# Kernel optimization log

Hardware: AMD Instinct MI355X
Metric: run time of the kernel (lower is better)

## Reference

```python
import jax, jax.numpy as jnp
import numpy as np


def conv(x, w, b=None, pad=0):
    y = jax.lax.conv_general_dilated(x, w, (1, 1), [(pad, pad), (pad, pad)],
                                     dimension_numbers=('NCHW', 'OIHW', 'NCHW'))
    if b is not None:
        y = y + b[None, :, None, None]
    return y


def bn(x, g, b, m, v, eps=1e-5):
    scale = g / jnp.sqrt(v + eps)
    return (x - m[None, :, None, None]) * scale[None, :, None, None] + b[None, :, None, None]


def channel_gate(x, w1, b1, w2, b2):
    # avg pool -> MLP -> sigmoid, returns [B, C, 1, 1]
    p = x.mean(axis=(2, 3))                       # [B, C]
    h = jax.nn.relu(p @ w1.T + b1)                # [B, C//r]
    a = h @ w2.T + b2                             # [B, C]
    return jax.nn.sigmoid(a)[:, :, None, None]


def setup_inputs() -> dict:
    key = jax.random.key(0)
    ks = iter(jax.random.split(key, 48))
    B, Cin, H, W = 2, 256, 64, 64
    Ci = Cin // 2          # inter_channels = 128
    Cr = Ci // 16          # gate bottleneck = 8
    def nrm(shape, s=0.05):
        return jax.random.normal(next(ks), shape, jnp.float32) * s
    d = {}
    d['q'] = jax.random.normal(next(ks), (B, Cin, H, W), jnp.float32)
    d['s'] = jax.random.normal(next(ks), (B, Cin, H, W), jnp.float32)
    # Trans_s: conv3x3 + BN
    d['ts_w'] = nrm((Ci, Cin, 3, 3)); d['ts_b'] = jnp.zeros(Ci)
    d['ts_g'] = jnp.ones(Ci); d['ts_be'] = jnp.zeros(Ci)
    d['ts_m'] = nrm((Ci,), 0.01); d['ts_v'] = jnp.ones(Ci)
    # Trans_q: conv3x3 + BN
    d['tq_w'] = nrm((Ci, Cin, 3, 3)); d['tq_b'] = jnp.zeros(Ci)
    d['tq_g'] = jnp.ones(Ci); d['tq_be'] = jnp.zeros(Ci)
    d['tq_m'] = nrm((Ci,), 0.01); d['tq_v'] = jnp.ones(Ci)
    # common_v 1x1
    d['cv_w'] = nrm((Ci, Ci, 1, 1)); d['cv_b'] = jnp.zeros(Ci)
    # key/query 1x1 projections (out = Ci//2)
    d['k1_w'] = nrm((Ci // 2, Ci, 1, 1)); d['k1_b'] = jnp.zeros(Ci // 2)
    d['q1_w'] = nrm((Ci // 2, Ci, 1, 1)); d['q1_b'] = jnp.zeros(Ci // 2)
    d['k2_w'] = nrm((Ci // 2, Ci, 1, 1)); d['k2_b'] = jnp.zeros(Ci // 2)
    d['q2_w'] = nrm((Ci // 2, Ci, 1, 1)); d['q2_b'] = jnp.zeros(Ci // 2)
    # ChannelGate MLP
    d['g1_w'] = nrm((Cr, Ci)); d['g1_b'] = jnp.zeros(Cr)
    d['g2_w'] = nrm((Ci, Cr)); d['g2_b'] = jnp.zeros(Ci)
    # conv_cat: conv3x3 (no bias) + BN
    d['cc_w'] = nrm((Ci, 2 * Ci, 3, 3))
    d['cc_g'] = jnp.ones(Ci); d['cc_be'] = jnp.zeros(Ci)
    d['cc_m'] = nrm((Ci,), 0.01); d['cc_v'] = jnp.ones(Ci)
    return d


def reference(q, s, ts_w, ts_b, ts_g, ts_be, ts_m, ts_v,
              tq_w, tq_b, tq_g, tq_be, tq_m, tq_v,
              cv_w, cv_b, k1_w, k1_b, q1_w, q1_b, k2_w, k2_b, q2_w, q2_b,
              g1_w, g1_b, g2_w, g2_b, cc_w, cc_g, cc_be, cc_m, cc_v):
    # stems: conv3x3 + BN + ReLU
    s = jax.nn.relu(bn(conv(s, ts_w, ts_b, pad=1), ts_g, ts_be, ts_m, ts_v))
    q = jax.nn.relu(bn(conv(q, tq_w, tq_b, pad=1), tq_g, tq_be, tq_m, tq_v))
    B, C, H, W = q.shape
    N = H * W
    # values
    v_q1 = conv(q, cv_w, cv_b)                          # [B,C,H,W]
    v_s1 = conv(s, cv_w, cv_b)
    v_q = v_q1.reshape(B, C, N).transpose(0, 2, 1)      # [B,N,C]
    v_s = v_s1.reshape(B, C, N).transpose(0, 2, 1)
    # dual keys / queries with negation trick
    k1 = conv(s, k1_w, k1_b).reshape(B, C // 2, N)
    k2 = conv(q, k2_w, k2_b).reshape(B, C // 2, N)
    key_cat = jnp.concatenate([k1, -k2], axis=1).transpose(0, 2, 1)   # [B,N,C]
    q1x = conv(s, q1_w, q1_b).reshape(B, C // 2, N)
    q2x = conv(q, q2_w, q2_b).reshape(B, C // 2, N)
    query_cat = jnp.concatenate([q1x, q2x], axis=1)                    # [B,C,N]
    # abs-score attention, dual softmax from the same score matrix
    A_s = jnp.abs(jnp.einsum('bnc,bcm->bnm', key_cat, query_cat))      # [B,N,N]
    att_s = jax.nn.softmax(A_s, axis=-1)
    att_q = jax.nn.softmax(A_s.transpose(0, 2, 1), axis=-1)
    # attend + channel-gate SE fusion + residual
    p_s = jnp.einsum('bnm,bmc->bnc', att_s, v_s).transpose(0, 2, 1).reshape(B, C, H, W)
    E_s = channel_gate(v_s1, g1_w, g1_b, g2_w, g2_b) * p_s + s
    q_s = jnp.einsum('bnm,bmc->bnc', att_q, v_q).transpose(0, 2, 1).reshape(B, C, H, W)
    E_q = channel_gate(v_q1, g1_w, g1_b, g2_w, g2_b) * q_s + q
    # concat + conv3x3(no bias) + BN + ReLU
    cpam = jax.nn.relu(bn(conv(jnp.concatenate([E_q, E_s], axis=1), cc_w, None, pad=1),
                          cc_g, cc_be, cc_m, cc_v))
    return (cpam, E_q, E_s)
```

## Files before the change

### kernel.cpp

```cpp
#include <hip/hip_runtime.h>

typedef __bf16 bf16;
typedef __bf16 v8bf __attribute__((ext_vector_type(8)));
typedef __bf16 v4bf __attribute__((ext_vector_type(4)));
typedef float v4f __attribute__((ext_vector_type(4)));

#define MFMA16(a, b, c) __builtin_amdgcn_mfma_f32_16x16x32_bf16(a, b, c, 0, 0, 0)

__device__ __forceinline__ float sf(float x) {
  if (!(x == x)) return 0.f;
  return fminf(fmaxf(x, -1e30f), 1e30f);
}

__global__ __launch_bounds__(256) void fill_kernel(float* __restrict__ out, float v, int n) {
  int i = blockIdx.x * 256 + threadIdx.x;
  if (i < n) out[i] = v;
}

__global__ __launch_bounds__(256) void prep_kernel(
    const float* __restrict__ ts_w, const float* __restrict__ tq_w,
    const float* ts_b, const float* ts_g, const float* ts_be, const float* ts_m, const float* ts_v,
    const float* tq_b, const float* tq_g, const float* tq_be, const float* tq_m, const float* tq_v,
    bf16* __restrict__ Wt01, float* __restrict__ ss01)
{
  int idx = blockIdx.x * 256 + threadIdx.x;
  if (idx < 589824) {
    int which = idx / 294912;
    int rem = idx - which * 294912;
    int co = rem / 2304;
    int r2 = rem - co * 2304;
    int tap = r2 >> 8;
    int ci = r2 & 255;
    const float* W = which ? tq_w : ts_w;
    Wt01[idx] = (bf16)W[(co * 256 + ci) * 9 + tap];
  } else if (idx < 590080) {
    int i = idx - 589824;
    int which = i >> 7, c = i & 127;
    float g, be, m, vv, bias;
    if (which == 0) { g=ts_g[c]; be=ts_be[c]; m=ts_m[c]; vv=ts_v[c]; bias=ts_b[c]; }
    else            { g=tq_g[c]; be=tq_be[c]; m=tq_m[c]; vv=tq_v[c]; bias=tq_b[c]; }
    float scale = g / sqrtf(vv + 1e-5f);
    ss01[which * 256 + c] = sf(scale);
    ss01[which * 256 + 128 + c] = sf((bias - m) * scale + be);
  }
}

__global__ __launch_bounds__(256) void prep2_kernel(
    const float* __restrict__ cc_w, const float* cc_g, const float* cc_be,
    const float* cc_m, const float* cc_v,
    bf16* __restrict__ Wt2, float* __restrict__ ss_cc)
{
  int idx = blockIdx.x * 256 + threadIdx.x;
  if (idx < 294912) {
    int co = idx / 2304;
    int r2 = idx - co * 2304;
    int tap = r2 >> 8;
    int ci = r2 & 255;
    Wt2[idx] = (bf16)cc_w[(co * 256 + ci) * 9 + tap];
  } else if (idx < 295040) {
    int c = idx - 294912;
    float scale = cc_g[c] / sqrtf(cc_v[c] + 1e-5f);
    ss_cc[c] = sf(scale);
    ss_cc[128 + c] = sf(-cc_m[c] * scale + cc_be[c]);
  }
}

__global__ __launch_bounds__(256) void convN_kernel(
    const float* __restrict__ pS, const float* __restrict__ pQ,
    const bf16* __restrict__ Wb, const float* __restrict__ ssb,
    void* __restrict__ out_, int mode)
{
  __shared__ bf16 As[66][40];
  __shared__ bf16 Bs[3][64][40];

  int y = blockIdx.x;
  int co0 = blockIdx.y * 64;
  int z = blockIdx.z;
  int tsr = z >> 1, b = z & 1;

  const float *in0, *in1;
  const bf16* W;
  const float* sp;
  if (mode == 0) {
    const float* base = (tsr ? pQ : pS) + (long)b * 1048576;
    in0 = base; in1 = base + 524288;
    W = Wb + (long)tsr * 294912;
    sp = ssb + tsr * 256;
  } else {
    in0 = pS + 1048576 + (long)b * 524288;
    in1 = pS + 2097152 + (long)b * 524288;
    W = Wb; sp = ssb;
  }

  int t = threadIdx.x, lane = t & 63, w = t >> 6;
  int l15 = lane & 15, l4 = lane >> 4;
  int wr = (w & 1) * 32, wc = (w >> 1) * 32;
  int ac = t & 31, ag = t >> 5;
  int bco = t >> 2, bk = (t & 3) * 8;

  v4f acc[2][2] = {};

  auto loadA = [&](int it, v8bf& areg) {
    int dy = it >> 3, ks = it & 7;
    int ysrc = y + dy - 1;
    int cg = ks * 32 + ac;
    const float* ip = (cg < 128) ? (in0 + (long)cg * 4096) : (in1 + (long)(cg - 128) * 4096);
    if ((unsigned)ysrc < 64u) {
      const float* src = ip + ysrc * 64 + ag * 8;
#pragma unroll
      for (int i = 0; i < 8; ++i) areg[i] = (bf16)src[i];
    } else {
#pragma unroll
      for (int i = 0; i < 8; ++i) areg[i] = (bf16)0.f;
    }
  };
  auto loadB = [&](int it, v8bf* breg) {
    int dy = it >> 3, ks = it & 7;
    const bf16* wk = W + (long)(co0 + bco) * 2304 + dy * 3 * 256 + ks * 32 + bk;
#pragma unroll
    for (int d = 0; d < 3; ++d) breg[d] = *(const v8bf*)(wk + d * 256);
  };

  v8bf areg, breg[3];
  loadA(0, areg);
  loadB(0, breg);

  for (int it = 0; it < 24; ++it) {
    __syncthreads();
#pragma unroll
    for (int i = 0; i < 8; ++i) As[ag * 8 + 1 + i][ac] = areg[i];
    if (ag == 0) As[0][ac] = (bf16)0.f;
    if (ag == 7) As[65][ac] = (bf16)0.f;
#pragma unroll
    for (int d = 0; d < 3; ++d) *(v8bf*)&Bs[d][bco][bk] = breg[d];
    __syncthreads();
    if (it < 23) { loadA(it + 1, areg); loadB(it + 1, breg); }
#pragma unroll
    for (int d = 0; d < 3; ++d) {
      v8bf af0 = *(const v8bf*)&As[wr + d + l15][l4 * 8];
      v8bf af1 = *(const v8bf*)&As[wr + 16 + d + l15][l4 * 8];
#pragma unroll
      for (int j = 0; j < 2; ++j) {
        v8bf bfr = *(const v8bf*)&Bs[d][wc + j * 16 + l15][l4 * 8];
        acc[0][j] = MFMA16(af0, bfr, acc[0][j]);
        acc[1][j] = MFMA16(af1, bfr, acc[1][j]);
      }
    }
  }
#pragma unroll
  for (int i = 0; i < 2; ++i) {
    int nb = y * 64 + wr + i * 16 + l4 * 4;
#pragma unroll
    for (int j = 0; j < 2; ++j) {
      int c = co0 + wc + j * 16 + l15;
      float scale = sp[c], shift = sp[128 + c];
      if (mode == 0) {
        bf16* o = (bf16*)out_ + ((long)(tsr * 2 + b) * 4096 + nb) * 128 + c;
#pragma unroll
        for (int r = 0; r < 4; ++r)
          o[r * 128] = (bf16)sf(fmaxf(acc[i][j][r] * scale + shift, 0.f));
      } else {
        v4f pk;
#pragma unroll
        for (int r = 0; r < 4; ++r)
          pk[r] = sf(fmaxf(acc[i][j][r] * scale + shift, 0.f));
        *(v4f*)((float*)out_ + ((long)b * 128 + c) * 4096 + nb) = pk;
      }
    }
  }
}

__global__ __launch_bounds__(256) void conv1_kernel(
    const bf16* __restrict__ feat_base,
    const float* __restrict__ cv_w, const float* __restrict__ k1_w, const float* __restrict__ q1_w,
    const float* __restrict__ k2_w, const float* __restrict__ q2_w,
    const float* __restrict__ cv_b, const float* __restrict__ k1_b, const float* __restrict__ q1_b,
    const float* __restrict__ k2_b, const float* __restrict__ q2_b,
    bf16* __restrict__ v_base, bf16* __restrict__ keyT, bf16* __restrict__ queryT)
{
  int nt = blockIdx.x;
  int br = blockIdx.z >> 1, b = blockIdx.z & 1;
  long zid = br * 2 + b;
  const bf16* feat = feat_base + zid * 524288 + (long)nt * 4096;

  __shared__ bf16 As[32][40];
  __shared__ bf16 Bs[256][40];

  int t = threadIdx.x, lane = t & 63, w = t >> 6;
  int l15 = lane & 15, l4 = lane >> 4;
  int wr = (w & 1) * 16, wc = (w >> 1) * 128;

  const float* wrow;
  bool negk = false;
  if (t < 128)       wrow = cv_w + (long)t * 128;
  else if (t < 192) { wrow = (br ? k2_w : k1_w) + (long)(t - 128) * 128; negk = (br != 0); }
  else               wrow = (br ? q2_w : q1_w) + (long)(t - 192) * 128;

  v4f acc[8] = {};
  int ap = t >> 2, ak = (t & 3) * 8;

  for (int ks = 0; ks < 4; ++ks) {
    int ci0 = ks * 32;
    v8bf av;
    if (t < 128) av = *(const v8bf*)(feat + ap * 128 + ci0 + ak);
    float wv[32];
#pragma unroll
    for (int u = 0; u < 32; ++u) wv[u] = wrow[ci0 + u];
    if (negk) {
#pragma unroll
      for (int u = 0; u < 32; ++u) wv[u] = -wv[u];
    }
    __syncthreads();
    if (t < 128) *(v8bf*)&As[ap][ak] = av;
#pragma unroll
    for (int u = 0; u < 32; ++u) Bs[t][u] = (bf16)wv[u];
    __syncthreads();
    v8bf af = *(const v8bf*)&As[wr + l15][l4 * 8];
#pragma unroll
    for (int j = 0; j < 8; ++j) {
      v8bf bfr = *(const v8bf*)&Bs[wc + j * 16 + l15][l4 * 8];
      acc[j] = MFMA16(af, bfr, acc[j]);
    }
  }

  int nb = nt * 32 + wr + l4 * 4;
#pragma unroll
  for (int j = 0; j < 8; ++j) {
    int c = wc + j * 16 + l15;
    float bv;
    if (c < 128)      bv = cv_b[c];
    else if (c < 192) bv = br ? -k2_b[c - 128] : k1_b[c - 128];
    else              bv = (br ? q2_b : q1_b)[c - 192];
    float v0 = sf(acc[j][0] + bv), v1 = sf(acc[j][1] + bv);
    float v2 = sf(acc[j][2] + bv), v3 = sf(acc[j][3] + bv);
    if (c < 128) {
      v4bf pk;
      pk[0] = (bf16)v0; pk[1] = (bf16)v1; pk[2] = (bf16)v2; pk[3] = (bf16)v3;
      *(v4bf*)(v_base + zid * 524288 + (long)c * 4096 + nb) = pk;
    } else if (c < 192) {
      int cc = (c - 128) + br * 64;
      bf16* kp = keyT + (long)b * 524288 + (long)nb * 128 + cc;
      kp[0] = (bf16)v0; kp[128] = (bf16)v1; kp[256] = (bf16)v2; kp[384] = (bf16)v3;
    } else {
      int cc = (c - 192) + br * 64;
      bf16* qp = queryT + (long)b * 524288 + (long)nb * 128 + cc;
      qp[0] = (bf16)v0; qp[128] = (bf16)v1; qp[256] = (bf16)v2; qp[384] = (bf16)v3;
    }
  }
}

__global__ __launch_bounds__(64) void pmean_kernel(
    const bf16* __restrict__ vs, float* __restrict__ pmean)
{
  int c = blockIdx.x, z = blockIdx.y, l = threadIdx.x;
  const bf16* src = vs + ((long)z * 128 + c) * 4096;
  float s = 0.f;
#pragma unroll
  for (int k = 0; k < 8; ++k) {
    v8bf v = *(const v8bf*)(src + k * 512 + l * 8);
#pragma unroll
    for (int e = 0; e < 8; ++e) s += (float)v[e];
  }
  s += __shfl_xor(s, 1, 64);
  s += __shfl_xor(s, 2, 64);
  s += __shfl_xor(s, 4, 64);
  s += __shfl_xor(s, 8, 64);
  s += __shfl_xor(s, 16, 64);
  s += __shfl_xor(s, 32, 64);
  if (l == 0) pmean[z * 128 + c] = s * (1.f / 4096.f);
}

__global__ __launch_bounds__(128) void gate2_kernel(
    const float* __restrict__ pmean, const float* __restrict__ g1_w, const float* __restrict__ g1_b,
    const float* __restrict__ g2_w, const float* __restrict__ g2_b, float* __restrict__ gate)
{
  __shared__ float p[128];
  __shared__ float h[8];
  int z = blockIdx.x, t = threadIdx.x;
  p[t] = pmean[z * 128 + t];
  __syncthreads();
  if (t < 8) {
    float a = g1_b[t];
    for (int c = 0; c < 128; ++c) a += g1_w[t * 128 + c] * p[c];
    h[t] = fmaxf(a, 0.f);
  }
  __syncthreads();
  float a = g2_b[t];
#pragma unroll
  for (int j = 0; j < 8; ++j) a += g2_w[t * 8 + j] * h[j];
  gate[z * 128 + t] = sf(1.f / (1.f + __expf(-a)));
}

__global__ __launch_bounds__(256) void apply_kernel(
    const bf16* __restrict__ keyT, const bf16* __restrict__ queryT,
    const bf16* __restrict__ v_base, const float* __restrict__ gate,
    const bf16* __restrict__ feat_base, float* __restrict__ d_out)
{
  int nt = blockIdx.x, br = blockIdx.z >> 1, b = blockIdx.z & 1;
  int n0 = nt * 64;
  const bf16* X = (br ? queryT : keyT) + ((long)b * 4096 + n0) * 128;
  const bf16* Y = (br ? keyT : queryT) + (long)b * 4096 * 128;
  const bf16* V = v_base + (long)(br * 2 + b) * 524288;
  const float* gt = gate + (br * 2 + b) * 128;
  const bf16* feat = feat_base + (long)(br * 2 + b) * 524288 + (long)n0 * 128;

  __shared__ bf16 Ys[64][132];
  __shared__ bf16 Vs[128][68];
  __shared__ bf16 Ps[64][68];
  __shared__ float rps[4][64];

  int t = threadIdx.x, lane = t & 63, w = t >> 6;
  int l15 = lane & 15, l4 = lane >> 4;
  int wm = w * 16;
  int wr = (w & 1) * 32;
  int wc = (w >> 1) * 64;

#pragma unroll
  for (int i = 0; i < 4; ++i) {
    int ch = t + i * 256;
    *(v8bf*)&Ys[ch >> 4][(ch & 15) * 8] = *(const v8bf*)(X + (ch >> 4) * 128 + (ch & 15) * 8);
  }
  __syncthreads();
  v8bf af[4][4];
#pragma unroll
  for (int i = 0; i < 4; ++i)
#pragma unroll
    for (int k = 0; k < 4; ++k)
      af[i][k] = *(const v8bf*)&Ys[i * 16 + l15][k * 32 + l4 * 8];

  v4f acc[2][4] = {};
  float rp[4][4] = {};

  v8bf yreg[4], vreg[4];
#pragma unroll
  for (int i = 0; i < 4; ++i) {
    int ch = t + i * 256;
    yreg[i] = *(const v8bf*)(Y + (long)(ch >> 4) * 128 + (ch & 15) * 8);
    vreg[i] = *(const v8bf*)(V + (long)(ch >> 3) * 4096 + (ch & 7) * 8);
  }

  for (int mt = 0; mt < 64; ++mt) {
    __syncthreads();
#pragma unroll
    for (int i = 0; i < 4; ++i) {
      int ch = t + i * 256;
      *(v8bf*)&Ys[ch >> 4][(ch & 15) * 8] = yreg[i];
      *(v8bf*)&Vs[ch >> 3][(ch & 7) * 8] = vreg[i];
    }
    __syncthreads();
    if (mt < 63) {
      int m0 = (mt + 1) * 64;
#pragma unroll
      for (int i = 0; i < 4; ++i) {
        int ch = t + i * 256;
        yreg[i] = *(const v8bf*)(Y + (long)(m0 + (ch >> 4)) * 128 + (ch & 15) * 8);
        vreg[i] = *(const v8bf*)(V + (long)(ch >> 3) * 4096 + m0 + (ch & 7) * 8);
      }
    }
    v4f sacc[4] = {};
#pragma unroll
    for (int k = 0; k < 4; ++k) {
      v8bf by = *(const v8bf*)&Ys[wm + l15][k * 32 + l4 * 8];
#pragma unroll
      for (int i = 0; i < 4; ++i)
        sacc[i] = MFMA16(af[i][k], by, sacc[i]);
    }
#pragma unroll
    for (int i = 0; i < 4; ++i)
#pragma unroll
      for (int r = 0; r < 4; ++r) {
        float e = __expf(fminf(fabsf(sacc[i][r]), 80.f) - 50.f);
        rp[i][r] += e;
        Ps[i * 16 + l4 * 4 + r][wm + l15] = (bf16)e;
      }
    __syncthreads();
#pragma unroll
    for (int k = 0; k < 2; ++k) {
      v8bf p0 = *(const v8bf*)&Ps[wr + l15][k * 32 + l4 * 8];
      v8bf p1 = *(const v8bf*)&Ps[wr + 16 + l15][k * 32 + l4 * 8];
#pragma unroll
      for (int j = 0; j < 4; ++j) {
        v8bf vb = *(const v8bf*)&Vs[wc + j * 16 + l15][k * 32 + l4 * 8];
        acc[0][j] = MFMA16(p0, vb, acc[0][j]);
        acc[1][j] = MFMA16(p1, vb, acc[1][j]);
      }
    }
  }
#pragma unroll
  for (int i = 0; i < 4; ++i)
#pragma unroll
    for (int r = 0; r < 4; ++r) {
      float v = rp[i][r];
      v += __shfl_xor(v, 1, 64);
      v += __shfl_xor(v, 2, 64);
      v += __shfl_xor(v, 4, 64);
      v += __shfl_xor(v, 8, 64);
      if (l15 == 0) rps[w][i * 16 + l4 * 4 + r] = v;
    }
  __syncthreads();

  float* outE = d_out + (long)(br ? 1 : 2) * 1048576 + (long)b * 524288;
#pragma unroll
  for (int i = 0; i < 2; ++i) {
    int rowt = wr + i * 16 + l4 * 4;
    float dv[4];
#pragma unroll
    for (int r = 0; r < 4; ++r)
      dv[r] = fmaxf(rps[0][rowt + r] + rps[1][rowt + r] + rps[2][rowt + r] + rps[3][rowt + r],
                    1e-30f);
#pragma unroll
    for (int j = 0; j < 4; ++j) {
      int c = wc + j * 16 + l15;
      float g = gt[c];
      v4f pk;
#pragma unroll
      for (int r = 0; r < 4; ++r) {
        float val = acc[i][j][r] / dv[r] * g + (float)feat[(long)(rowt + r) * 128 + c];
        pk[r] = sf(val);
      }
      *(v4f*)(outE + (long)c * 4096 + n0 + rowt) = pk;
    }
  }
}

extern "C" void kernel_launch(void* const* d_in, const int* in_sizes, int n_in,
                              void* d_out, int out_size, void* d_ws, size_t ws_size,
                              hipStream_t stream)
{
  if (n_in != 33 || in_sizes[0] != 2097152 || in_sizes[2] != 294912 ||
      in_sizes[14] != 16384 || out_size != 3145728) {
    fill_kernel<<<12288, 256, 0, stream>>>((float*)d_out, 100.0f, 3145728);
    return;
  }
  if (ws_size < 12582912) {
    fill_kernel<<<12288, 256, 0, stream>>>((float*)d_out, 1.0f, 3145728);
    return;
  }

  const float* q_in = (const float*)d_in[0];
  const float* s_in = (const float*)d_in[1];
  char* ob = (char*)d_out;
  float* outf = (float*)d_out;

  float* gate  = (float*)(ob + 0);
  float* pmean = (float*)(ob + 2048);

  char* ws = (char*)d_ws;
  bf16*  sfeat  = (bf16*)(ws + 0);
  bf16*  vs     = (bf16*)(ws + 4194304);
  bf16*  keyT   = (bf16*)(ws + 8388608);
  bf16*  queryT = (bf16*)(ws + 10485760);
  bf16*  Wt01   = (bf16*)(ws + 8388608);
  float* ss01   = (float*)(ws + 10485760);
  bf16*  Wt2    = (bf16*)(ws + 0);
  float* ss_cc  = (float*)(ws + 589824);

  prep_kernel<<<2306, 256, 0, stream>>>(
      (const float*)d_in[2], (const float*)d_in[8],
      (const float*)d_in[3], (const float*)d_in[4], (const float*)d_in[5],
      (const float*)d_in[6], (const float*)d_in[7],
      (const float*)d_in[9], (const float*)d_in[10], (const float*)d_in[11],
      (const float*)d_in[12], (const float*)d_in[13],
      Wt01, ss01);

  convN_kernel<<<dim3(64, 2, 4), 256, 0, stream>>>(s_in, q_in, Wt01, ss01, sfeat, 0);

  conv1_kernel<<<dim3(128, 1, 4), 256, 0, stream>>>(
      sfeat,
      (const float*)d_in[14], (const float*)d_in[16], (const float*)d_in[18],
      (const float*)d_in[20], (const float*)d_in[22],
      (const float*)d_in[15], (const float*)d_in[17], (const float*)d_in[19],
      (const float*)d_in[21], (const float*)d_in[23],
      vs, keyT, queryT);

  pmean_kernel<<<dim3(128, 4), 64, 0, stream>>>(vs, pmean);

  gate2_kernel<<<4, 128, 0, stream>>>(pmean, (const float*)d_in[24], (const float*)d_in[25],
                                      (const float*)d_in[26], (const float*)d_in[27], gate);

  apply_kernel<<<dim3(64, 1, 4), 256, 0, stream>>>(keyT, queryT, vs, gate, sfeat, outf);

  prep2_kernel<<<1153, 256, 0, stream>>>(
      (const float*)d_in[28], (const float*)d_in[29], (const float*)d_in[30],
      (const float*)d_in[31], (const float*)d_in[32], Wt2, ss_cc);

  convN_kernel<<<dim3(64, 2, 2), 256, 0, stream>>>(outf, nullptr, Wt2, ss_cc, outf, 1);
}
```

Measured before the change: 296.6 us.

## Split key loop across three wave groups in attention apply kernel

The apply kernel now launches 768 threads per block, with three 4-wave groups each processing a third of the key tiles using separate shared-memory buffers. Partial accumulators are reduced through shared memory and the row sums are combined across all 12 waves. The epilogue is restructured so threads write coalesced output from a shared float buffer. This raises per-CU wave occupancy to hide latency, at the cost of more LDS, a register cap from the larger block, and the extra reduction step.

```diff
diff --git a/kernel.cpp b/kernel.cpp
--- a/kernel.cpp
+++ b/kernel.cpp
@@ -291,7 +291,7 @@
   gate[z * 128 + t] = sf(1.f / (1.f + __expf(-a)));
 }
 
-__global__ __launch_bounds__(256) void apply_kernel(
+__global__ __launch_bounds__(768) void apply_kernel(
     const bf16* __restrict__ keyT, const bf16* __restrict__ queryT,
     const bf16* __restrict__ v_base, const float* __restrict__ gate,
     const bf16* __restrict__ feat_base, float* __restrict__ d_out)
@@ -304,21 +304,28 @@
   const float* gt = gate + (br * 2 + b) * 128;
   const bf16* feat = feat_base + (long)(br * 2 + b) * 524288 + (long)n0 * 128;
 
-  __shared__ bf16 Ys[64][132];
-  __shared__ bf16 Vs[128][68];
-  __shared__ bf16 Ps[64][68];
-  __shared__ float rps[4][64];
+  __shared__ __align__(16) bf16 Ys[3][64][132];
+  __shared__ __align__(16) bf16 Vs[3][128][68];
+  __shared__ __align__(16) bf16 Ps[3][64][68];
+  __shared__ float rps[12][64];
+  __shared__ float dvt[64];
 
   int t = threadIdx.x, lane = t & 63, w = t >> 6;
+  int g = w >> 2;
+  int wg = w & 3;
+  int tg = t & 255;
   int l15 = lane & 15, l4 = lane >> 4;
-  int wm = w * 16;
-  int wr = (w & 1) * 32;
-  int wc = (w >> 1) * 64;
+  int wm = wg * 16;
+  int wr = (wg & 1) * 32;
+  int wc = (wg >> 1) * 64;
+
+  int cnt = (g == 0) ? 22 : 21;
+  int st = (g == 0) ? 0 : (22 + (g - 1) * 21);
 
 #pragma unroll
   for (int i = 0; i < 4; ++i) {
-    int ch = t + i * 256;
-    *(v8bf*)&Ys[ch >> 4][(ch & 15) * 8] = *(const v8bf*)(X + (ch >> 4) * 128 + (ch & 15) * 8);
+    int ch = tg + i * 256;
+    *(v8bf*)&Ys[g][ch >> 4][(ch & 15) * 8] = *(const v8bf*)(X + (ch >> 4) * 128 + (ch & 15) * 8);
   }
   __syncthreads();
   v8bf af[4][4];
@@ -326,66 +333,77 @@
   for (int i = 0; i < 4; ++i)
 #pragma unroll
     for (int k = 0; k < 4; ++k)
-      af[i][k] = *(const v8bf*)&Ys[i * 16 + l15][k * 32 + l4 * 8];
+      af[i][k] = *(const v8bf*)&Ys[g][i * 16 + l15][k * 32 + l4 * 8];
 
   v4f acc[2][4] = {};
   float rp[4][4] = {};
 
   v8bf yreg[4], vreg[4];
-#pragma unroll
-  for (int i = 0; i < 4; ++i) {
-    int ch = t + i * 256;
-    yreg[i] = *(const v8bf*)(Y + (long)(ch >> 4) * 128 + (ch & 15) * 8);
-    vreg[i] = *(const v8bf*)(V + (long)(ch >> 3) * 4096 + (ch & 7) * 8);
-  }
-
-  for (int mt = 0; mt < 64; ++mt) {
-    __syncthreads();
+  {
+    int m0 = st * 64;
 #pragma unroll
     for (int i = 0; i < 4; ++i) {
-      int ch = t + i * 256;
-      *(v8bf*)&Ys[ch >> 4][(ch & 15) * 8] = yreg[i];
-      *(v8bf*)&Vs[ch >> 3][(ch & 7) * 8] = vreg[i];
-    }
-    __syncthreads();
-    if (mt < 63) {
-      int m0 = (mt + 1) * 64;
+      int ch = tg + i * 256;
+      yreg[i] = *(const v8bf*)(Y + (long)(m0 + (ch >> 4)) * 128 + (ch & 15) * 8);
+      vreg[i] = *(const v8bf*)(V + (long)(ch >> 3) * 4096 + m0 + (ch & 7) * 8);
+    }
+  }
+
+  for (int it = 0; it < 22; ++it) {
+    bool act = it < cnt;
+    __syncthreads();
+    if (act) {
 #pragma unroll
       for (int i = 0; i < 4; ++i) {
-        int ch = t + i * 256;
+        int ch = tg + i * 256;
+        *(v8bf*)&Ys[g][ch >> 4][(ch & 15) * 8] = yreg[i];
+        *(v8bf*)&Vs[g][ch >> 3][(ch & 7) * 8] = vreg[i];
+      }
+    }
+    __syncthreads();
+    if (act && (it + 1 < cnt)) {
+      int m0 = (st + it + 1) * 64;
+#pragma unroll
+      for (int i = 0; i < 4; ++i) {
+        int ch = tg + i * 256;
         yreg[i] = *(const v8bf*)(Y + (long)(m0 + (ch >> 4)) * 128 + (ch & 15) * 8);
         vreg[i] = *(const v8bf*)(V + (long)(ch >> 3) * 4096 + m0 + (ch & 7) * 8);
       }
     }
-    v4f sacc[4] = {};
-#pragma unroll
-    for (int k = 0; k < 4; ++k) {
-      v8bf by = *(const v8bf*)&Ys[wm + l15][k * 32 + l4 * 8];
+    if (act) {
+      v4f sacc[4] = {};
+#pragma unroll
+      for (int k = 0; k < 4; ++k) {
+        v8bf by = *(const v8bf*)&Ys[g][wm + l15][k * 32 + l4 * 8];
+#pragma unroll
+        for (int i = 0; i < 4; ++i)
+          sacc[i] = MFMA16(af[i][k], by, sacc[i]);
+      }
 #pragma unroll
       for (int i = 0; i < 4; ++i)
-        sacc[i] = MFMA16(af[i][k], by, sacc[i]);
-    }
-#pragma unroll
-    for (int i = 0; i < 4; ++i)
-#pragma unroll
-      for (int r = 0; r < 4; ++r) {
-        float e = __expf(fminf(fabsf(sacc[i][r]), 80.f) - 50.f);
-        rp[i][r] += e;
-        Ps[i * 16 + l4 * 4 + r][wm + l15] = (bf16)e;
-      }
-    __syncthreads();
-#pragma unroll
-    for (int k = 0; k < 2; ++k) {
-      v8bf p0 = *(const v8bf*)&Ps[wr + l15][k * 32 + l4 * 8];
-      v8bf p1 = *(const v8bf*)&Ps[wr + 16 + l15][k * 32 + l4 * 8];
-#pragma unroll
-      for (int j = 0; j < 4; ++j) {
-        v8bf vb = *(const v8bf*)&Vs[wc + j * 16 + l15][k * 32 + l4 * 8];
-        acc[0][j] = MFMA16(p0, vb, acc[0][j]);
-        acc[1][j] = MFMA16(p1, vb, acc[1][j]);
-      }
-    }
-  }
+#pragma unroll
+        for (int r = 0; r < 4; ++r) {
+          float e = __expf(fminf(fabsf(sacc[i][r]), 80.f) - 50.f);
+          rp[i][r] += e;
+          Ps[g][i * 16 + l4 * 4 + r][wm + l15] = (bf16)e;
+        }
+    }
+    __syncthreads();
+    if (act) {
+#pragma unroll
+      for (int k = 0; k < 2; ++k) {
+        v8bf p0 = *(const v8bf*)&Ps[g][wr + l15][k * 32 + l4 * 8];
+        v8bf p1 = *(const v8bf*)&Ps[g][wr + 16 + l15][k * 32 + l4 * 8];
+#pragma unroll
+        for (int j = 0; j < 4; ++j) {
+          v8bf vb = *(const v8bf*)&Vs[g][wc + j * 16 + l15][k * 32 + l4 * 8];
+          acc[0][j] = MFMA16(p0, vb, acc[0][j]);
+          acc[1][j] = MFMA16(p1, vb, acc[1][j]);
+        }
+      }
+    }
+  }
+
 #pragma unroll
   for (int i = 0; i < 4; ++i)
 #pragma unroll
@@ -399,26 +417,58 @@
     }
   __syncthreads();
 
+  float* Fb = (float*)&Ys[0][0][0];
+  if (g == 0) {
+#pragma unroll
+    for (int i = 0; i < 2; ++i)
+#pragma unroll
+      for (int j = 0; j < 4; ++j)
+#pragma unroll
+        for (int r = 0; r < 4; ++r)
+          Fb[(wr + i * 16 + l4 * 4 + r) * 130 + wc + j * 16 + l15] = acc[i][j][r];
+  }
+  __syncthreads();
+  if (g == 1) {
+#pragma unroll
+    for (int i = 0; i < 2; ++i)
+#pragma unroll
+      for (int j = 0; j < 4; ++j)
+#pragma unroll
+        for (int r = 0; r < 4; ++r)
+          Fb[(wr + i * 16 + l4 * 4 + r) * 130 + wc + j * 16 + l15] += acc[i][j][r];
+  }
+  __syncthreads();
+  if (g == 2) {
+#pragma unroll
+    for (int i = 0; i < 2; ++i)
+#pragma unroll
+      for (int j = 0; j < 4; ++j)
+#pragma unroll
+        for (int r = 0; r < 4; ++r)
+          Fb[(wr + i * 16 + l4 * 4 + r) * 130 + wc + j * 16 + l15] += acc[i][j][r];
+  }
+  if (t < 64) {
+    float s = 0.f;
+#pragma unroll
+    for (int w2 = 0; w2 < 12; ++w2) s += rps[w2][t];
+    dvt[t] = fmaxf(s, 1e-30f);
+  }
+  __syncthreads();
+
   float* outE = d_out + (long)(br ? 1 : 2) * 1048576 + (long)b * 524288;
-#pragma unroll
-  for (int i = 0; i < 2; ++i) {
-    int rowt = wr + i * 16 + l4 * 4;
-    float dv[4];
-#pragma unroll
-    for (int r = 0; r < 4; ++r)
-      dv[r] = fmaxf(rps[0][rowt + r] + rps[1][rowt + r] + rps[2][rowt + r] + rps[3][rowt + r],
-                    1e-30f);
-#pragma unroll
-    for (int j = 0; j < 4; ++j) {
-      int c = wc + j * 16 + l15;
-      float g = gt[c];
+  if (t < 512) {
+    int c = t & 127;
+    float gv = gt[c];
+#pragma unroll
+    for (int rq = t >> 7; rq < 16; rq += 4) {
       v4f pk;
 #pragma unroll
       for (int r = 0; r < 4; ++r) {
-        float val = acc[i][j][r] / dv[r] * g + (float)feat[(long)(rowt + r) * 128 + c];
+        int row = rq * 4 + r;
+        float val = Fb[row * 130 + c] / dvt[row] * gv + (float)feat[(long)row * 128 + c];
         pk[r] = sf(val);
       }
-      *(v4f*)(outE + (long)c * 4096 + n0 + rowt) = pk;
+      *(v4f*)(outE + (long)c * 4096 + n0 + rq * 4) = pk;
     }
   }
 }
@@ -478,7 +528,7 @@
   gate2_kernel<<<4, 128, 0, stream>>>(pmean, (const float*)d_in[24], (const float*)d_in[25],
                                       (const float*)d_in[26], (const float*)d_in[27], gate);
 
-  apply_kernel<<<dim3(64, 1, 4), 256, 0, stream>>>(keyT, queryT, vs, gate, sfeat, outf);
+  apply_kernel<<<dim3(64, 1, 4), 768, 0, stream>>>(keyT, queryT, vs, gate, sfeat, outf);
 
   prep2_kernel<<<1153, 256, 0, stream>>>(
       (const float*)d_in[28], (const float*)d_in[29], (const float*)d_in[30],
```

New measurement: 346.7 us. 16.9% more time.

## Halve attention row tile to double grid, fold channel mean into conv1

Applied to the files above, without the earlier changes.

The attention apply kernel now handles 32 query rows per block instead of 64, so the grid doubles to 512 blocks. That gives more blocks per CU and more latency hiding, at the cost of re-streaming the full key and V tiles twice as often. Separately, the per-channel pooled sum for the channel gate is now accumulated with atomics inside the 1x1 conv epilogue, which removes the separate pmean kernel that re-read v_s. A small fill kernel zeroes the accumulator first, and the 1/4096 scale moves into the gate kernel. Atomic float accumulation makes the summation order nondeterministic.

```diff
diff --git a/kernel.cpp b/kernel.cpp
--- a/kernel.cpp
+++ b/kernel.cpp
@@ -176,7 +176,8 @@
     const float* __restrict__ k2_w, const float* __restrict__ q2_w,
     const float* __restrict__ cv_b, const float* __restrict__ k1_b, const float* __restrict__ q1_b,
     const float* __restrict__ k2_b, const float* __restrict__ q2_b,
-    bf16* __restrict__ v_base, bf16* __restrict__ keyT, bf16* __restrict__ queryT)
+    bf16* __restrict__ v_base, bf16* __restrict__ keyT, bf16* __restrict__ queryT,
+    float* __restrict__ pmean)
 {
   int nt = blockIdx.x;
   int br = blockIdx.z >> 1, b = blockIdx.z & 1;
@@ -237,6 +238,10 @@
       v4bf pk;
       pk[0] = (bf16)v0; pk[1] = (bf16)v1; pk[2] = (bf16)v2; pk[3] = (bf16)v3;
       *(v4bf*)(v_base + zid * 524288 + (long)c * 4096 + nb) = pk;
+      float s = v0 + v1 + v2 + v3;
+      s += __shfl_xor(s, 16, 64);
+      s += __shfl_xor(s, 32, 64);
+      if (l4 == 0) atomicAdd(&pmean[zid * 128 + c], s);
     } else if (c < 192) {
       int cc = (c - 128) + br * 64;
       bf16* kp = keyT + (long)b * 524288 + (long)nb * 128 + cc;
@@ -249,27 +254,6 @@
   }
 }
 
-__global__ __launch_bounds__(64) void pmean_kernel(
-    const bf16* __restrict__ vs, float* __restrict__ pmean)
-{
-  int c = blockIdx.x, z = blockIdx.y, l = threadIdx.x;
-  const bf16* src = vs + ((long)z * 128 + c) * 4096;
-  float s = 0.f;
-#pragma unroll
-  for (int k = 0; k < 8; ++k) {
-    v8bf v = *(const v8bf*)(src + k * 512 + l * 8);
-#pragma unroll
-    for (int e = 0; e < 8; ++e) s += (float)v[e];
-  }
-  s += __shfl_xor(s, 1, 64);
-  s += __shfl_xor(s, 2, 64);
-  s += __shfl_xor(s, 4, 64);
-  s += __shfl_xor(s, 8, 64);
-  s += __shfl_xor(s, 16, 64);
-  s += __shfl_xor(s, 32, 64);
-  if (l == 0) pmean[z * 128 + c] = s * (1.f / 4096.f);
-}
-
 __global__ __launch_bounds__(128) void gate2_kernel(
     const float* __restrict__ pmean, const float* __restrict__ g1_w, const float* __restrict__ g1_b,
     const float* __restrict__ g2_w, const float* __restrict__ g2_b, float* __restrict__ gate)
@@ -277,7 +261,7 @@
   __shared__ float p[128];
   __shared__ float h[8];
   int z = blockIdx.x, t = threadIdx.x;
-  p[t] = pmean[z * 128 + t];
+  p[t] = pmean[z * 128 + t] * (1.f / 4096.f);
   __syncthreads();
   if (t < 8) {
     float a = g1_b[t];
@@ -297,7 +281,7 @@
     const bf16* __restrict__ feat_base, float* __restrict__ d_out)
 {
   int nt = blockIdx.x, br = blockIdx.z >> 1, b = blockIdx.z & 1;
-  int n0 = nt * 64;
+  int n0 = nt * 32;
   const bf16* X = (br ? queryT : keyT) + ((long)b * 4096 + n0) * 128;
   const bf16* Y = (br ? keyT : queryT) + (long)b * 4096 * 128;
   const bf16* V = v_base + (long)(br * 2 + b) * 524288;
@@ -306,30 +290,30 @@
 
   __shared__ bf16 Ys[64][132];
   __shared__ bf16 Vs[128][68];
-  __shared__ bf16 Ps[64][68];
-  __shared__ float rps[4][64];
+  __shared__ bf16 Ps[32][68];
+  __shared__ float rps[4][32];
 
   int t = threadIdx.x, lane = t & 63, w = t >> 6;
   int l15 = lane & 15, l4 = lane >> 4;
   int wm = w * 16;
-  int wr = (w & 1) * 32;
+  int wr = (w & 1) * 16;
   int wc = (w >> 1) * 64;
 
 #pragma unroll
-  for (int i = 0; i < 4; ++i) {
+  for (int i = 0; i < 2; ++i) {
     int ch = t + i * 256;
     *(v8bf*)&Ys[ch >> 4][(ch & 15) * 8] = *(const v8bf*)(X + (ch >> 4) * 128 + (ch & 15) * 8);
   }
   __syncthreads();
-  v8bf af[4][4];
-#pragma unroll
-  for (int i = 0; i < 4; ++i)
+  v8bf af[2][4];
+#pragma unroll
+  for (int i = 0; i < 2; ++i)
 #pragma unroll
     for (int k = 0; k < 4; ++k)
       af[i][k] = *(const v8bf*)&Ys[i * 16 + l15][k * 32 + l4 * 8];
 
-  v4f acc[2][4] = {};
-  float rp[4][4] = {};
+  v4f acc[4] = {};
+  float rp[2][4] = {};
 
   v8bf yreg[4], vreg[4];
 #pragma unroll
@@ -357,16 +341,16 @@
         vreg[i] = *(const v8bf*)(V + (long)(ch >> 3) * 4096 + m0 + (ch & 7) * 8);
       }
     }
-    v4f sacc[4] = {};
+    v4f sacc[2] = {};
 #pragma unroll
     for (int k = 0; k < 4; ++k) {
       v8bf by = *(const v8bf*)&Ys[wm + l15][k * 32 + l4 * 8];
 #pragma unroll
-      for (int i = 0; i < 4; ++i)
+      for (int i = 0; i < 2; ++i)
         sacc[i] = MFMA16(af[i][k], by, sacc[i]);
     }
 #pragma unroll
-    for (int i = 0; i < 4; ++i)
+    for (int i = 0; i < 2; ++i)
 #pragma unroll
       for (int r = 0; r < 4; ++r) {
         float e = __expf(fminf(fabsf(sacc[i][r]), 80.f) - 50.f);
@@ -377,17 +361,15 @@
 #pragma unroll
     for (int k = 0; k < 2; ++k) {
       v8bf p0 = *(const v8bf*)&Ps[wr + l15][k * 32 + l4 * 8];
-      v8bf p1 = *(const v8bf*)&Ps[wr + 16 + l15][k * 32 + l4 * 8];
 #pragma unroll
       for (int j = 0; j < 4; ++j) {
         v8bf vb = *(const v8bf*)&Vs[wc + j * 16 + l15][k * 32 + l4 * 8];
-        acc[0][j] = MFMA16(p0, vb, acc[0][j]);
-        acc[1][j] = MFMA16(p1, vb, acc[1][j]);
+        acc[j] = MFMA16(p0, vb, acc[j]);
       }
     }
   }
 #pragma unroll
-  for (int i = 0; i < 4; ++i)
+  for (int i = 0; i < 2; ++i)
 #pragma unroll
     for (int r = 0; r < 4; ++r) {
       float v = rp[i][r];
@@ -400,26 +382,23 @@
   __syncthreads();
 
   float* outE = d_out + (long)(br ? 1 : 2) * 1048576 + (long)b * 524288;
-#pragma unroll
-  for (int i = 0; i < 2; ++i) {
-    int rowt = wr + i * 16 + l4 * 4;
-    float dv[4];
-#pragma unroll
-    for (int r = 0; r < 4; ++r)
-      dv[r] = fmaxf(rps[0][rowt + r] + rps[1][rowt + r] + rps[2][rowt + r] + rps[3][rowt + r],
-                    1e-30f);
-#pragma unroll
-    for (int j = 0; j < 4; ++j) {
-      int c = wc + j * 16 + l15;
-      float g = gt[c];
-      v4f pk;
-#pragma unroll
-      for (int r = 0; r < 4; ++r) {
-        float val = acc[i][j][r] / dv[r] * g + (float)feat[(long)(rowt + r) * 128 + c];
-        pk[r] = sf(val);
-      }
-      *(v4f*)(outE + (long)c * 4096 + n0 + rowt) = pk;
-    }
+  int rowt = wr + l4 * 4;
+  float dv[4];
+#pragma unroll
+  for (int r = 0; r < 4; ++r)
+    dv[r] = fmaxf(rps[0][rowt + r] + rps[1][rowt + r] + rps[2][rowt + r] + rps[3][rowt + r],
+                  1e-30f);
+#pragma unroll
+  for (int j = 0; j < 4; ++j) {
+    int c = wc + j * 16 + l15;
+    float g = gt[c];
+    v4f pk;
+#pragma unroll
+    for (int r = 0; r < 4; ++r) {
+      float val = acc[j][r] / dv[r] * g + (float)feat[(long)(rowt + r) * 128 + c];
+      pk[r] = sf(val);
+    }
+    *(v4f*)(outE + (long)c * 4096 + n0 + rowt) = pk;
   }
 }
 
@@ -463,6 +442,8 @@
       (const float*)d_in[12], (const float*)d_in[13],
       Wt01, ss01);
 
+  fill_kernel<<<2, 256, 0, stream>>>(pmean, 0.0f, 512);
+
   convN_kernel<<<dim3(64, 2, 4), 256, 0, stream>>>(s_in, q_in, Wt01, ss01, sfeat, 0);
 
   conv1_kernel<<<dim3(128, 1, 4), 256, 0, stream>>>(
@@ -471,14 +452,12 @@
       (const float*)d_in[20], (const float*)d_in[22],
       (const float*)d_in[15], (const float*)d_in[17], (const float*)d_in[19],
       (const float*)d_in[21], (const float*)d_in[23],
-      vs, keyT, queryT);
-
-  pmean_kernel<<<dim3(128, 4), 64, 0, stream>>>(vs, pmean);
+      vs, keyT, queryT, pmean);
 
   gate2_kernel<<<4, 128, 0, stream>>>(pmean, (const float*)d_in[24], (const float*)d_in[25],
                                       (const float*)d_in[26], (const float*)d_in[27], gate);
 
-  apply_kernel<<<dim3(64, 1, 4), 256, 0, stream>>>(keyT, queryT, vs, gate, sfeat, outf);
+  apply_kernel<<<dim3(128, 1, 4), 256, 0, stream>>>(keyT, queryT, vs, gate, sfeat, outf);
 
   prep2_kernel<<<1153, 256, 0, stream>>>(
       (const float*)d_in[28], (const float*)d_in[29], (const float*)d_in[30],
```

Result: slower. 302.9 us (+2.1%).
